# Kernel optimization log

Hardware: AMD Instinct MI355X
Metric: run time of the kernel (lower is better)

Reference implementation:

```python
import jax, jax.numpy as jnp
import numpy as np

NUM_EMBEDDINGS = 1024
EMBEDDING_DIM = 256
COMMITMENT_COST = 0.25
DECAY = 0.99
EPS = 1e-5


def setup_inputs() -> dict:
    key = jax.random.key(0)
    k0, k1, k2 = jax.random.split(key, 3)
    x = jax.random.normal(k0, (32, 2048, EMBEDDING_DIM), dtype=jnp.float32)
    # embedding.weight.data.uniform_(-1/K, 1/K)
    embedding_w = jax.random.uniform(
        k1, (NUM_EMBEDDINGS, EMBEDDING_DIM), dtype=jnp.float32,
        minval=-1.0 / NUM_EMBEDDINGS, maxval=1.0 / NUM_EMBEDDINGS)
    ema_cluster_size = jnp.zeros((NUM_EMBEDDINGS,), dtype=jnp.float32)
    ema_w = jax.random.normal(k2, (NUM_EMBEDDINGS, EMBEDDING_DIM), dtype=jnp.float32)
    return {"x": x, "embedding_w": embedding_w,
            "ema_cluster_size": ema_cluster_size, "ema_w": ema_w}


def reference(x, embedding_w, ema_cluster_size, ema_w):
    K, D = embedding_w.shape
    flat = x.reshape(-1, D)  # [N, D]

    # squared L2 distances to codebook: [N, K]
    distances = ((flat * flat).sum(axis=1, keepdims=True)
                 - 2.0 * flat @ embedding_w.T
                 + (embedding_w * embedding_w).sum(axis=1))
    indices = jnp.argmin(distances, axis=1)  # [N] int

    # gather quantized vectors
    quantized = embedding_w[indices].reshape(x.shape)

    # EMA statistics via scatter-add (one-hot.T @ flat without materializing one-hot)
    counts = jax.ops.segment_sum(jnp.ones((flat.shape[0],), dtype=flat.dtype),
                                 indices, num_segments=K)  # [K]
    dw = jax.ops.segment_sum(flat, indices, num_segments=K)  # [K, D]

    new_cluster_size = DECAY * ema_cluster_size + (1.0 - DECAY) * counts
    new_ema_w = DECAY * ema_w + (1.0 - DECAY) * dw

    # Laplace smoothing of cluster sizes, normalized codebook update
    n = new_cluster_size.sum()
    cs = (new_cluster_size + EPS) / (n + K * EPS) * n
    new_embedding_w = new_ema_w / cs[:, None]

    # commitment loss (codebook side is EMA-updated, so only e-latent term)
    e_latent_loss = jnp.mean((jax.lax.stop_gradient(quantized) - x) ** 2)
    loss = COMMITMENT_COST * e_latent_loss

    # straight-through estimator
    quantized_st = x + jax.lax.stop_gradient(quantized - x)

    avg_probs = counts / counts.sum()
    perplexity = jnp.exp(-jnp.sum(avg_probs * jnp.log(avg_probs + 1e-10)))

    return (loss, quantized_st, perplexity,
            new_embedding_w, new_cluster_size, new_ema_w)
```

## Files before the change

### kernel.cpp

```cpp
#include <hip/hip_runtime.h>
#include <math.h>

#define N_ROWS   65536
#define K_EMB    1024
#define D_EMB    256

typedef __attribute__((ext_vector_type(8)))  short short8;
typedef __attribute__((ext_vector_type(4)))  short short4v;
typedef __attribute__((ext_vector_type(16))) float floatx16;

__device__ inline unsigned short f2bf(float f) {
    unsigned u = __float_as_uint(f);
    unsigned r = u + 0x7fffu + ((u >> 16) & 1u);
    return (unsigned short)(r >> 16);
}
__device__ inline float bf2f(unsigned short s) {
    return __uint_as_float(((unsigned)s) << 16);
}

__global__ __launch_bounds__(64)
void prep_e(const float* __restrict__ ew, float* __restrict__ half_esq,
            short* __restrict__ pack_hi, short* __restrict__ pack_lo,
            int* __restrict__ counts, double* __restrict__ loss_buckets)
{
    const int k = blockIdx.x;
    const int t = threadIdx.x;

    if (t == 0) {
        counts[k] = 0;
        if (k < 256) loss_buckets[k] = 0.0;
    }

    float4 v = *(const float4*)(ew + (size_t)k * D_EMB + t * 4);
    float s = v.x * v.x + v.y * v.y + v.z * v.z + v.w * v.w;
#pragma unroll
    for (int off = 32; off > 0; off >>= 1) s += __shfl_down(s, off);
    if (t == 0) half_esq[k] = 0.5f * s;

    const int d0   = t * 4;
    const int tile = k >> 5;
    const int kt   = d0 >> 4;
    const int half = (d0 & 15) >> 3;
    const int lane = (k & 31) + 32 * half;
    const int j0   = d0 & 7;
    const int off  = tile * 8192 + kt * 512 + lane * 8 + j0;

    float f[4] = {-v.x, -v.y, -v.z, -v.w};
    short4v h, l;
#pragma unroll
    for (int j = 0; j < 4; ++j) {
        unsigned short hh = f2bf(f[j]);
        h[j] = (short)hh;
        l[j] = (short)f2bf(f[j] - bf2f(hh));
    }
    *(short4v*)(pack_hi + off) = h;
    *(short4v*)(pack_lo + off) = l;
}

__global__ __launch_bounds__(256, 2)
void argmin_mfma(const float* __restrict__ x,
                 const short* __restrict__ pack_hi,
                 const short* __restrict__ pack_lo,
                 const float* __restrict__ half_esq,
                 const float* __restrict__ ew,
                 int* __restrict__ indices,
                 float* __restrict__ out_q,
                 double* __restrict__ loss_buckets,
                 int* __restrict__ counts)
{
    __shared__ short xs_hi[32 * 256];
    __shared__ short xs_lo[32 * 256];
    __shared__ float cmv[128];
    __shared__ int   cmi[128];
    __shared__ int   widx[32];

    const int t  = threadIdx.x;
    const int r0 = blockIdx.x * 32;

#pragma unroll
    for (int i = 0; i < 4; ++i) {
        int q   = i * 256 + t;
        int row = q >> 5;
        int g8  = q & 31;
        const float* gp = x + (size_t)(r0 + row) * D_EMB + g8 * 8;
        float4 a = *(const float4*)gp;
        float4 b = *(const float4*)(gp + 4);
        float f[8] = {a.x, a.y, a.z, a.w, b.x, b.y, b.z, b.w};
        short8 h8, l8;
#pragma unroll
        for (int j = 0; j < 8; ++j) {
            unsigned short hh = f2bf(f[j]);
            h8[j] = (short)hh;
            l8[j] = (short)f2bf(f[j] - bf2f(hh));
        }
        int off = row * 256 + ((g8 ^ (row & 7)) << 3);
        *(short8*)(xs_hi + off) = h8;
        *(short8*)(xs_lo + off) = l8;
    }
    __syncthreads();

    const int w    = t >> 6;
    const int lane = t & 63;
    const int l31  = lane & 31;
    const int half = lane >> 5;
    const int key  = l31 & 7;
    const short* bbase_h = xs_hi + l31 * 256;
    const short* bbase_l = xs_lo + l31 * 256;

    float mv = 3.4e38f;
    int   mi = 0;

    for (int cp = 0; cp < 4; ++cp) {
        const int c0 = w * 256 + cp * 64;
        const int c1 = c0 + 32;
        const int tile0 = c0 >> 5;

        floatx16 acc0, acc1;
#pragma unroll
        for (int rq = 0; rq < 4; ++rq) {
            float4 e0 = *(const float4*)(half_esq + c0 + rq * 8 + half * 4);
            float4 e1 = *(const float4*)(half_esq + c1 + rq * 8 + half * 4);
            acc0[rq * 4 + 0] = e0.x; acc0[rq * 4 + 1] = e0.y;
            acc0[rq * 4 + 2] = e0.z; acc0[rq * 4 + 3] = e0.w;
            acc1[rq * 4 + 0] = e1.x; acc1[rq * 4 + 1] = e1.y;
            acc1[rq * 4 + 2] = e1.z; acc1[rq * 4 + 3] = e1.w;
        }

        const short* p0h = pack_hi + tile0 * 8192 + lane * 8;
        const short* p0l = pack_lo + tile0 * 8192 + lane * 8;
        const short* p1h = p0h + 8192;
        const short* p1l = p0l + 8192;

        short8 a0h = *(const short8*)(p0h);
        short8 a0l = *(const short8*)(p0l);
        short8 a1h = *(const short8*)(p1h);
        short8 a1l = *(const short8*)(p1l);

#pragma unroll 4
        for (int kt = 0; kt < 16; ++kt) {
            short8 n0h, n0l, n1h, n1l;
            if (kt < 15) {
                n0h = *(const short8*)(p0h + (kt + 1) * 512);
                n0l = *(const short8*)(p0l + (kt + 1) * 512);
                n1h = *(const short8*)(p1h + (kt + 1) * 512);
                n1l = *(const short8*)(p1l + (kt + 1) * 512);
            }
            int coff = (((2 * kt + half) ^ key) << 3);
            short8 bh = *(const short8*)(bbase_h + coff);
            short8 bl = *(const short8*)(bbase_l + coff);
            acc0 = __builtin_amdgcn_mfma_f32_32x32x16_bf16(a0h, bh, acc0, 0, 0, 0);
            acc1 = __builtin_amdgcn_mfma_f32_32x32x16_bf16(a1h, bh, acc1, 0, 0, 0);
            acc0 = __builtin_amdgcn_mfma_f32_32x32x16_bf16(a0h, bl, acc0, 0, 0, 0);
            acc1 = __builtin_amdgcn_mfma_f32_32x32x16_bf16(a1h, bl, acc1, 0, 0, 0);
            acc0 = __builtin_amdgcn_mfma_f32_32x32x16_bf16(a0l, bh, acc0, 0, 0, 0);
            acc1 = __builtin_amdgcn_mfma_f32_32x32x16_bf16(a1l, bh, acc1, 0, 0, 0);
            a0h = n0h; a0l = n0l; a1h = n1h; a1l = n1l;
        }

#pragma unroll
        for (int r = 0; r < 16; ++r) {
            int code0 = c0 + (r & 3) + ((r >> 2) << 3) + half * 4;
            float v0 = acc0[r];
            if (v0 < mv || (v0 == mv && code0 < mi)) { mv = v0; mi = code0; }
            int code1 = code0 + 32;
            float v1 = acc1[r];
            if (v1 < mv || (v1 == mv && code1 < mi)) { mv = v1; mi = code1; }
        }
    }

    {
        float ov = __shfl_xor(mv, 32);
        int   oi = __shfl_xor(mi, 32);
        if (ov < mv || (ov == mv && oi < mi)) { mv = ov; mi = oi; }
    }

    if (half == 0) {
        int slot = w * 32 + l31;
        cmv[slot] = mv;
        cmi[slot] = mi;
    }
    __syncthreads();
    if (t < 32) {
        float bv = cmv[t];
        int   bi = cmi[t];
#pragma unroll
        for (int ww = 1; ww < 4; ++ww) {
            float v = cmv[ww * 32 + t];
            int   i = cmi[ww * 32 + t];
            if (v < bv || (v == bv && i < bi)) { bv = v; bi = i; }
        }
        indices[r0 + t] = bi;
        widx[t] = bi;
        atomicAdd(&counts[bi], 1);
    }
    __syncthreads();

    const int g8e  = lane >> 1;
    const int j0e  = (lane & 1) * 4;
    float lsum = 0.0f;
#pragma unroll
    for (int rr = 0; rr < 8; ++rr) {
        const int row = w * 8 + rr;
        const int idx = widx[row];
        const int off = row * 256 + (((g8e) ^ (row & 7)) << 3) + j0e;
        short4v h4 = *(const short4v*)(xs_hi + off);
        short4v l4 = *(const short4v*)(xs_lo + off);
        float xr[4];
#pragma unroll
        for (int j = 0; j < 4; ++j)
            xr[j] = bf2f((unsigned short)h4[j]) + bf2f((unsigned short)l4[j]);
        const float4 ev = *(const float4*)(ew + (size_t)idx * D_EMB + lane * 4);
        float4 q;
        q.x = xr[0] + (ev.x - xr[0]);
        q.y = xr[1] + (ev.y - xr[1]);
        q.z = xr[2] + (ev.z - xr[2]);
        q.w = xr[3] + (ev.w - xr[3]);
        *(float4*)(out_q + (size_t)(r0 + row) * D_EMB + lane * 4) = q;
        float dx = ev.x - xr[0], dy = ev.y - xr[1];
        float dz = ev.z - xr[2], dwv = ev.w - xr[3];
        lsum += dx * dx + dy * dy + dz * dz + dwv * dwv;
    }
#pragma unroll
    for (int off = 32; off > 0; off >>= 1) lsum += __shfl_down(lsum, off);
    if (lane == 0) atomicAdd(&loss_buckets[blockIdx.x & 255], (double)lsum);
}

__global__ __launch_bounds__(1024)
void finalize_small(const float* __restrict__ ema_cs,
                    const int* __restrict__ counts,
                    const double* __restrict__ loss_buckets,
                    float* __restrict__ cs_ws,
                    float* __restrict__ out_loss,
                    float* __restrict__ out_perp,
                    float* __restrict__ out_ncs,
                    int* __restrict__ offsets,
                    int* __restrict__ cursor)
{
    __shared__ float  red[1024];
    __shared__ double redd[256];
    __shared__ int    sc[1024];
    const int k = threadIdx.x;
    const int icnt = counts[k];
    const float cnt = (float)icnt;
    const float ncs = 0.99f * ema_cs[k] + 0.01f * cnt;
    out_ncs[k] = ncs;
    red[k] = ncs;
    sc[k]  = icnt;
    __syncthreads();
    for (int off = 512; off > 0; off >>= 1) {
        if (k < off) red[k] += red[k + off];
        __syncthreads();
    }
    const float n = red[0];
    __syncthreads();
    cs_ws[k] = (ncs + 1e-5f) / (n + 1024.0f * 1e-5f) * n;

    for (int d = 1; d < 1024; d <<= 1) {
        int add = (k >= d) ? sc[k - d] : 0;
        __syncthreads();
        sc[k] += add;
        __syncthreads();
    }
    offsets[k] = sc[k] - icnt;
    cursor[k]  = 0;

    const float p = cnt / 65536.0f;
    red[k] = p * logf(p + 1e-10f);
    if (k < 256) redd[k] = loss_buckets[k];
    __syncthreads();
    for (int off = 512; off > 0; off >>= 1) {
        if (k < off) red[k] += red[k + off];
        __syncthreads();
    }
    if (k == 0) out_perp[0] = expf(-red[0]);
    for (int off = 128; off > 0; off >>= 1) {
        if (k < off) redd[k] += redd[k + off];
        __syncthreads();
    }
    if (k == 0) out_loss[0] = (float)(0.25 * (redd[0] / 16777216.0));
}

__global__ __launch_bounds__(256)
void scatter_rows(const int* __restrict__ indices,
                  const int* __restrict__ offsets,
                  int* __restrict__ cursor,
                  int* __restrict__ row_sorted)
{
    const int row = blockIdx.x * 256 + threadIdx.x;
    const int idx = indices[row];
    const int pos = atomicAdd(&cursor[idx], 1);
    row_sorted[offsets[idx] + pos] = row;
}

__global__ __launch_bounds__(256)
void gather_update(const float* __restrict__ x,
                   const int* __restrict__ row_sorted,
                   const int* __restrict__ offsets,
                   const int* __restrict__ counts,
                   const float* __restrict__ ema_w,
                   const float* __restrict__ cs_ws,
                   float* __restrict__ out_emb,
                   float* __restrict__ out_ema)
{
    __shared__ int rows[2048];
    const int k   = blockIdx.x;
    const int t   = threadIdx.x;
    const int off = offsets[k];
    const int cnt = counts[k];
    float sum = 0.0f;

    for (int c = 0; c < cnt; c += 2048) {
        const int m = min(cnt - c, 2048);
        for (int i = t; i < m; i += 256) rows[i] = row_sorted[off + c + i];
        __syncthreads();
        int r = 0;
        for (; r + 4 <= m; r += 4) {
            int i0 = rows[r], i1 = rows[r + 1], i2 = rows[r + 2], i3 = rows[r + 3];
            float v0 = x[(size_t)i0 * D_EMB + t];
            float v1 = x[(size_t)i1 * D_EMB + t];
            float v2 = x[(size_t)i2 * D_EMB + t];
            float v3 = x[(size_t)i3 * D_EMB + t];
            sum += (v0 + v1) + (v2 + v3);
        }
        for (; r < m; ++r)
            sum += x[(size_t)rows[r] * D_EMB + t];
        __syncthreads();
    }

    const size_t o = (size_t)k * D_EMB + t;
    const float nev = 0.99f * ema_w[o] + 0.01f * sum;
    out_ema[o] = nev;
    out_emb[o] = nev / cs_ws[k];
}

extern "C" void kernel_launch(void* const* d_in, const int* in_sizes, int n_in,
                              void* d_out, int out_size, void* d_ws, size_t ws_size,
                              hipStream_t stream)
{
    const float* x       = (const float*)d_in[0];
    const float* ew      = (const float*)d_in[1];
    const float* ema_cs  = (const float*)d_in[2];
    const float* ema_w   = (const float*)d_in[3];

    float* out       = (float*)d_out;
    float* out_loss  = out;
    float* out_q     = out + 1;
    float* out_perp  = out + 1 + 16777216;
    float* out_emb   = out_perp + 1;
    float* out_ncs   = out_emb + 262144;
    float* out_ema   = out_ncs + 1024;

    char* ws = (char*)d_ws;
    int*    counts       = (int*)(ws);
    double* loss_buckets = (double*)(ws + 4096);
    float*  half_esq     = (float*)(ws + 6144);
    float*  cs_ws        = (float*)(ws + 10240);
    int*    offsets      = (int*)(ws + 14336);
    int*    cursor       = (int*)(ws + 18432);
    int*    indices      = (int*)(ws + 22528);
    int*    row_sorted   = (int*)(ws + 284672);

    short* pack_hi = (short*)(out + 16777220);
    short* pack_lo = (short*)(out + 16777220 + 131072);

    prep_e<<<K_EMB, 64, 0, stream>>>(ew, half_esq, pack_hi, pack_lo,
                                     counts, loss_buckets);
    argmin_mfma<<<N_ROWS / 32, 256, 0, stream>>>(x, pack_hi, pack_lo, half_esq,
                                                 ew, indices, out_q, loss_buckets,
                                                 counts);
    finalize_small<<<1, 1024, 0, stream>>>(ema_cs, counts, loss_buckets, cs_ws,
                                           out_loss, out_perp, out_ncs,
                                           offsets, cursor);
    scatter_rows<<<N_ROWS / 256, 256, 0, stream>>>(indices, offsets, cursor,
                                                   row_sorted);
    gather_update<<<K_EMB, 256, 0, stream>>>(x, row_sorted, offsets, counts,
                                             ema_w, cs_ws, out_emb, out_ema);
}
```

Measured before the change: 264.4 us.

## Use 8 waves per argmin block and move count histogram to separate kernel

The argmin kernel now runs 512 threads per block, so each of 8 waves scans 128 codebook entries instead of 256. Launch bounds request 8 blocks per CU to raise occupancy and latency hiding. The per-row global atomic on cluster counts moves out of the argmin kernel into a new histogram kernel that bins indices in shared memory, adding one extra launch. The tighter launch bound may force register spills in the MFMA accumulation loop.

```diff
diff --git a/kernel.cpp b/kernel.cpp
--- a/kernel.cpp
+++ b/kernel.cpp
@@ -57,7 +57,7 @@
     *(short4v*)(pack_lo + off) = l;
 }
 
-__global__ __launch_bounds__(256, 2)
+__global__ __launch_bounds__(512, 8)
 void argmin_mfma(const float* __restrict__ x,
                  const short* __restrict__ pack_hi,
                  const short* __restrict__ pack_lo,
@@ -65,21 +65,20 @@
                  const float* __restrict__ ew,
                  int* __restrict__ indices,
                  float* __restrict__ out_q,
-                 double* __restrict__ loss_buckets,
-                 int* __restrict__ counts)
+                 double* __restrict__ loss_buckets)
 {
     __shared__ short xs_hi[32 * 256];
     __shared__ short xs_lo[32 * 256];
-    __shared__ float cmv[128];
-    __shared__ int   cmi[128];
+    __shared__ float cmv[256];
+    __shared__ int   cmi[256];
     __shared__ int   widx[32];
 
     const int t  = threadIdx.x;
     const int r0 = blockIdx.x * 32;
 
 #pragma unroll
-    for (int i = 0; i < 4; ++i) {
-        int q   = i * 256 + t;
+    for (int i = 0; i < 2; ++i) {
+        int q   = i * 512 + t;
         int row = q >> 5;
         int g8  = q & 31;
         const float* gp = x + (size_t)(r0 + row) * D_EMB + g8 * 8;
@@ -110,8 +109,8 @@
     float mv = 3.4e38f;
     int   mi = 0;
 
-    for (int cp = 0; cp < 4; ++cp) {
-        const int c0 = w * 256 + cp * 64;
+    for (int cp = 0; cp < 2; ++cp) {
+        const int c0 = w * 128 + cp * 64;
         const int c1 = c0 + 32;
         const int tile0 = c0 >> 5;
 
@@ -184,14 +183,13 @@
         float bv = cmv[t];
         int   bi = cmi[t];
 #pragma unroll
-        for (int ww = 1; ww < 4; ++ww) {
+        for (int ww = 1; ww < 8; ++ww) {
             float v = cmv[ww * 32 + t];
             int   i = cmi[ww * 32 + t];
             if (v < bv || (v == bv && i < bi)) { bv = v; bi = i; }
         }
         indices[r0 + t] = bi;
         widx[t] = bi;
-        atomicAdd(&counts[bi], 1);
     }
     __syncthreads();
 
@@ -199,8 +197,8 @@
     const int j0e  = (lane & 1) * 4;
     float lsum = 0.0f;
 #pragma unroll
-    for (int rr = 0; rr < 8; ++rr) {
-        const int row = w * 8 + rr;
+    for (int rr = 0; rr < 4; ++rr) {
+        const int row = w * 4 + rr;
         const int idx = widx[row];
         const int off = row * 256 + (((g8e) ^ (row & 7)) << 3) + j0e;
         short4v h4 = *(const short4v*)(xs_hi + off);
@@ -225,6 +223,29 @@
     if (lane == 0) atomicAdd(&loss_buckets[blockIdx.x & 255], (double)lsum);
 }
 
+__global__ __launch_bounds__(256)
+void histogram(const int* __restrict__ indices, int* __restrict__ counts)
+{
+    __shared__ int h[1024];
+    const int t = threadIdx.x;
+#pragma unroll
+    for (int i = 0; i < 4; ++i) h[i * 256 + t] = 0;
+    __syncthreads();
+    const int base = blockIdx.x * 4096 + t * 16;
+#pragma unroll
+    for (int i = 0; i < 4; ++i) {
+        int4 v = *(const int4*)(indices + base + i * 4);
+        atomicAdd(&h[v.x], 1); atomicAdd(&h[v.y], 1);
+        atomicAdd(&h[v.z], 1); atomicAdd(&h[v.w], 1);
+    }
+    __syncthreads();
+#pragma unroll
+    for (int i = 0; i < 4; ++i) {
+        int c = h[i * 256 + t];
+        if (c) atomicAdd(&counts[i * 256 + t], c);
+    }
+}
+
 __global__ __launch_bounds__(1024)
 void finalize_small(const float* __restrict__ ema_cs,
                     const int* __restrict__ counts,
@@ -365,9 +386,9 @@
 
     prep_e<<<K_EMB, 64, 0, stream>>>(ew, half_esq, pack_hi, pack_lo,
                                      counts, loss_buckets);
-    argmin_mfma<<<N_ROWS / 32, 256, 0, stream>>>(x, pack_hi, pack_lo, half_esq,
-                                                 ew, indices, out_q, loss_buckets,
-                                                 counts);
+    argmin_mfma<<<N_ROWS / 32, 512, 0, stream>>>(x, pack_hi, pack_lo, half_esq,
+                                                 ew, indices, out_q, loss_buckets);
+    histogram<<<16, 256, 0, stream>>>(indices, counts);
     finalize_small<<<1, 1024, 0, stream>>>(ema_cs, counts, loss_buckets, cs_ws,
                                            out_loss, out_perp, out_ncs,
                                            offsets, cursor);
```

Measured after the change: 837.1 us. 217% more time.
